# Performance work log

Measured on AMD Instinct MI355X. Metric: run time of the kernel, lower is better.

Reference implementation:

```python
import jax, jax.numpy as jnp
import numpy as np

N_NODES = 50000
N_EDGES = 1600000
N_GRAPHS = 64


def _gcn_conv(x, row, col, ew, W, b, n_nodes):
    # x: [N, Fin] -> [N, Fout]; PyG GCNConv: lin, add self-loops (w=1),
    # symmetric normalization, scatter-add at target (col), + bias.
    x = x @ W
    loop = jnp.arange(n_nodes, dtype=row.dtype)
    r = jnp.concatenate([row, loop])
    c = jnp.concatenate([col, loop])
    w = jnp.concatenate([ew, jnp.ones((n_nodes,), dtype=ew.dtype)])
    deg = jax.ops.segment_sum(w, c, num_segments=n_nodes)
    dinv = jnp.where(deg > 0, jax.lax.rsqrt(jnp.where(deg > 0, deg, 1.0)), 0.0)
    norm = dinv[r] * w * dinv[c]                      # [E+N]
    msg = x[r] * norm[:, None]                        # [E+N, Fout] (dominant traffic)
    out = jax.ops.segment_sum(msg, c, num_segments=n_nodes)
    return out + b


def setup_inputs() -> dict:
    key = jax.random.key(0)
    ks = jax.random.split(key, 12)
    x = jax.random.normal(ks[0], (N_NODES, 128), dtype=jnp.float32)
    edge_index = jax.random.randint(ks[1], (2, N_EDGES), 0, N_NODES, dtype=jnp.int32)
    edge_attr = jax.random.uniform(ks[2], (N_EDGES,), dtype=jnp.float32)
    batch = jnp.sort(jax.random.randint(ks[3], (N_NODES,), 0, N_GRAPHS, dtype=jnp.int32))
    glorot = lambda k, fi, fo: jax.random.normal(k, (fi, fo), jnp.float32) * np.sqrt(2.0 / (fi + fo))
    return {
        "x": x, "edge_index": edge_index, "edge_attr": edge_attr, "batch": batch,
        "W1": glorot(ks[4], 128, 128), "b1": jnp.zeros((128,), jnp.float32),
        "W2": glorot(ks[5], 128, 64), "b2": jnp.zeros((64,), jnp.float32),
        "fc1_W": glorot(ks[6], 64, 128), "fc1_b": jnp.zeros((128,), jnp.float32),
        "fc2_W": glorot(ks[7], 128, 2), "fc2_b": jnp.zeros((2,), jnp.float32),
    }


def reference(x, edge_index, edge_attr, batch, W1, b1, W2, b2, fc1_W, fc1_b, fc2_W, fc2_b):
    row, col = edge_index[0], edge_index[1]
    h = jax.nn.relu(_gcn_conv(x, row, col, edge_attr, W1, b1, N_NODES))
    x1 = jax.nn.relu(_gcn_conv(h, row, col, edge_attr, W2, b2, N_NODES))
    # global mean pool over batch ids
    sums = jax.ops.segment_sum(x1, batch, num_segments=N_GRAPHS)
    cnt = jax.ops.segment_sum(jnp.ones((N_NODES,), x1.dtype), batch, num_segments=N_GRAPHS)
    x2 = sums / jnp.maximum(cnt, 1.0)[:, None]        # [B, 64]
    # dropout is identity in eval mode
    h = jax.nn.relu(x2 @ fc1_W + fc1_b)
    logits = h @ fc2_W + fc2_b                        # [B, 2]
    return jax.nn.log_softmax(logits, axis=1)
```

## Files before the change

kernel.cpp:

```cpp
#include <hip/hip_runtime.h>
#include <hip/hip_bf16.h>


#define CAP 64
#define OVFCAP 8192
#define MAXNR 6400
#define PCH 32
#define BSTR 68
#define KP 136
#define PARTNB 256

typedef float v2f  __attribute__((ext_vector_type(2)));
typedef float f32x4 __attribute__((ext_vector_type(4)));
typedef short bf16x8 __attribute__((ext_vector_type(8)));

__device__ inline unsigned short f2bf(float f) {
    unsigned u = __float_as_uint(f);
    u += 0x7FFFu + ((u >> 16) & 1u);
    return (unsigned short)(u >> 16);
}
__device__ inline void fp8x4_to_f32(unsigned w, float* o) {
    v2f lo = __builtin_amdgcn_cvt_pk_f32_fp8((int)w, false);
    v2f hi = __builtin_amdgcn_cvt_pk_f32_fp8((int)w, true);
    o[0] = lo[0]; o[1] = lo[1]; o[2] = hi[0]; o[3] = hi[1];
}
__device__ inline unsigned f32x4_to_fp8(float a, float b, float c, float d) {
    int w = 0;
    w = __builtin_amdgcn_cvt_pk_fp8_f32(a, b, w, false);
    w = __builtin_amdgcn_cvt_pk_fp8_f32(c, d, w, true);
    return (unsigned)w;
}

__global__ void part_kernel(const int* __restrict__ rows, const int* __restrict__ cols,
                            const float* __restrict__ ew, int* __restrict__ rangeCnt,
                            uint2* __restrict__ rng, int E, int NR, int RSEG,
                            const float* __restrict__ W1, const float* __restrict__ W2,
                            unsigned short* __restrict__ wt1, unsigned short* __restrict__ wt2) {
    const int t = threadIdx.x;
    if (blockIdx.x >= PARTNB) {
        if (blockIdx.x == PARTNB) {
            for (int i = t; i < 128 * 128; i += 256) {
                int c = i >> 7, k = i & 127;
                wt1[c * KP + k] = f2bf(W1[k * 128 + c]);
            }
        } else {
            for (int i = t; i < 64 * 128; i += 256) {
                int c = i >> 7, k = i & 127;
                wt2[c * KP + k] = f2bf(W2[k * 64 + c]);
            }
        }
        return;
    }
    __shared__ int hc[8];
    const int CS = (E + PARTNB - 1) / PARTNB;
    const int e0 = blockIdx.x * CS, e1 = min(e0 + CS, E);
    if (t < 8) hc[t] = 0;
    __syncthreads();
    for (int e = e0 + t; e < e1; e += 256) {
        int r = cols[e] / NR;
        atomicAdd(&hc[r], 1);
    }
    __syncthreads();
    if (t < 8) hc[t] = atomicAdd(&rangeCnt[t], hc[t]);
    __syncthreads();
    for (int e = e0 + t; e < e1; e += 256) {
        int c = cols[e];
        int r = c / NR;
        int q = (int)(ew[e] * 32768.0f);
        if (q > 32767) q = 32767;
        unsigned rec = ((unsigned)rows[e] << 15) | (unsigned)q;
        int pos = atomicAdd(&hc[r], 1);
        if (pos < RSEG) rng[(size_t)r * RSEG + pos] = make_uint2((unsigned)c, rec);
    }
}

__global__ __launch_bounds__(1024)
void hist2_kernel(const uint2* __restrict__ rng, const int* __restrict__ rangeCnt,
                  int* __restrict__ h2d, int* __restrict__ w2d, int NR, int RSEG) {
    __shared__ int hist[MAXNR];
    __shared__ int wsum[MAXNR];
    const int r = blockIdx.x & 7, j = blockIdx.x >> 3;
    const int t = threadIdx.x;
    const int M = min(rangeCnt[r], RSEG);
    const int CS = (M + PCH - 1) / PCH;
    const int e0 = j * CS, e1 = min(e0 + CS, M);
    for (int n = t; n < NR; n += 1024) { hist[n] = 0; wsum[n] = 0; }
    __syncthreads();
    const uint2* lst = rng + (size_t)r * RSEG;
    for (int k = e0 + t; k < e1; k += 1024) {
        unsigned c = lst[k].x - r * NR;
        atomicAdd(&hist[c], 1);
        atomicAdd(&wsum[c], (int)(lst[k].y & 32767u));
    }
    __syncthreads();
    int* dst = h2d + (size_t)(r * PCH + j) * NR;
    int* wdst = w2d + (size_t)(r * PCH + j) * NR;
    for (int n = t; n < NR; n += 1024) { dst[n] = hist[n]; wdst[n] = wsum[n]; }
}

__global__ void scan2_kernel(int* __restrict__ h2d, const int* __restrict__ w2d,
                             int* __restrict__ cnt, float* __restrict__ dinv, int NR, int N) {
    int n = blockIdx.x * 256 + threadIdx.x;
    if (n >= N) return;
    int r = n / NR, c = n - r * NR;
    int* col = h2d + (size_t)(r * PCH) * NR + c;
    const int* wcol = w2d + (size_t)(r * PCH) * NR + c;
    int run = 0;
    long long ws = 0;
    #pragma unroll 8
    for (int j = 0; j < PCH; ++j) {
        int v = col[(size_t)j * NR];
        col[(size_t)j * NR] = run;
        run += v;
        ws += wcol[(size_t)j * NR];
    }
    cnt[n] = run;
    dinv[n] = rsqrtf((float)ws * (1.0f / 32768.0f) + 1.0f);
}

__global__ __launch_bounds__(1024)
void place2_kernel(const uint2* __restrict__ rng, const int* __restrict__ rangeCnt,
                   const int* __restrict__ h2d, unsigned* __restrict__ slot,
                   int4* __restrict__ ovf, int* __restrict__ ovfcnt,
                   int NR, int RSEG) {
    __shared__ int cur[MAXNR];
    const int r = blockIdx.x & 7, j = blockIdx.x >> 3;
    const int t = threadIdx.x;
    const int M = min(rangeCnt[r], RSEG);
    const int CS = (M + PCH - 1) / PCH;
    const int e0 = j * CS, e1 = min(e0 + CS, M);
    const int* src = h2d + (size_t)(r * PCH + j) * NR;
    for (int n = t; n < NR; n += 1024) cur[n] = src[n];
    __syncthreads();
    const uint2* lst = rng + (size_t)r * RSEG;
    for (int k = e0 + t; k < e1; k += 1024) {
        uint2 u2 = lst[k];
        int pos = atomicAdd(&cur[u2.x - r * NR], 1);
        if (pos < CAP) {
            slot[(size_t)u2.x * CAP + pos] = u2.y;
        } else {
            int o = atomicAdd(ovfcnt, 1);
            if (o < OVFCAP)
                ovf[o] = make_int4((int)(u2.y >> 15), (int)u2.x, (int)(u2.y & 32767u), 0);
        }
    }
}

__global__ void place_simple_kernel(const int* __restrict__ rows, const int* __restrict__ cols,
                                    const float* __restrict__ ew, int* __restrict__ cnt,
                                    unsigned* __restrict__ slot, int4* __restrict__ ovf,
                                    int* __restrict__ ovfcnt, int E) {
    int e = blockIdx.x * 256 + threadIdx.x;
    if (e >= E) return;
    int r = rows[e], c = cols[e];
    int q = (int)(ew[e] * 32768.0f);
    if (q > 32767) q = 32767;
    int pos = atomicAdd(&cnt[c], 1);
    if (pos < CAP) {
        slot[(size_t)c * CAP + pos] = ((unsigned)r << 15) | (unsigned)q;
    } else {
        int o = atomicAdd(ovfcnt, 1);
        if (o < OVFCAP) ovf[o] = make_int4(r, c, q, 0);
    }
}

__global__ void degfin_kernel(const unsigned* __restrict__ slot, const int* __restrict__ cnt,
                              const int4* __restrict__ ovf, const int* __restrict__ ovfcnt,
                              float* __restrict__ dinv, int N) {
    const int w = threadIdx.x >> 6, lane = threadIdx.x & 63;
    const int i = blockIdx.x * 4 + w;
    if (i >= N) return;
    int mraw = cnt[i];
    int m = mraw > CAP ? CAP : mraw;
    float v = 0.f;
    if (lane < m) v = (float)(slot[(size_t)i * CAP + lane] & 32767u);
    if (mraw > CAP) {
        int oc = *ovfcnt; if (oc > OVFCAP) oc = OVFCAP;
        for (int k = lane; k < oc; k += 64)
            if (ovf[k].y == i) v += (float)ovf[k].z;
    }
    #pragma unroll
    for (int off = 1; off < 64; off <<= 1) v += __shfl_xor(v, off);
    if (lane == 0) dinv[i] = rsqrtf(v * (1.0f / 32768.0f) + 1.0f);
}

template <int BN, bool AF32>
__global__ __launch_bounds__(256)
void gemm_mfma_kernel(const void* __restrict__ Av, const unsigned short* __restrict__ wt,
                      const float* __restrict__ dinv, unsigned char* __restrict__ outf8,
                      int M) {
    constexpr int CT = BN / 16;
    constexpr int EPS = BN + 4;
    __shared__ unsigned short wl[BN * KP];
    __shared__ float ep[4][16 * EPS];
    const int t = threadIdx.x;
    for (int i = t; i < BN * KP / 8; i += 256)
        ((uint4*)wl)[i] = ((const uint4*)wt)[i];
    __syncthreads();
    const int w = t >> 6, lane = t & 63;
    const int n16 = lane & 15, q = lane >> 4;
    const int rowBase = blockIdx.x * 64 + w * 16;
    int arow = rowBase + n16; if (arow >= M) arow = M - 1;
    f32x4 acc[CT];
    #pragma unroll
    for (int ct = 0; ct < CT; ++ct) acc[ct] = (f32x4){0.f, 0.f, 0.f, 0.f};
    #pragma unroll
    for (int kt = 0; kt < 4; ++kt) {
        bf16x8 af;
        if (AF32) {
            const float* ap = (const float*)Av + (size_t)arow * 128 + kt * 32 + q * 8;
            float4 a0 = *(const float4*)ap;
            float4 a1 = *(const float4*)(ap + 4);
            af[0] = (short)f2bf(a0.x); af[1] = (short)f2bf(a0.y);
            af[2] = (short)f2bf(a0.z); af[3] = (short)f2bf(a0.w);
            af[4] = (short)f2bf(a1.x); af[5] = (short)f2bf(a1.y);
            af[6] = (short)f2bf(a1.z); af[7] = (short)f2bf(a1.w);
        } else {
            af = *(const bf16x8*)((const unsigned short*)Av + (size_t)arow * 128 + kt * 32 + q * 8);
        }
        #pragma unroll
        for (int ct = 0; ct < CT; ++ct) {
            bf16x8 bfr = *(const bf16x8*)&wl[(ct * 16 + n16) * KP + kt * 32 + q * 8];
            acc[ct] = __builtin_amdgcn_mfma_f32_16x16x32_bf16(af, bfr, acc[ct], 0, 0, 0);
        }
    }
    #pragma unroll
    for (int ct = 0; ct < CT; ++ct)
        #pragma unroll
        for (int r = 0; r < 4; ++r)
            ep[w][(q * 4 + r) * EPS + ct * 16 + n16] = acc[ct][r];
    __syncthreads();
    const int lr = lane & 15;
    const int cc = (lane >> 4) * (BN / 4);
    int grow = rowBase + lr;
    if (grow < M) {
        float s = dinv[grow];
        const float* src = &ep[w][lr * EPS + cc];
        #pragma unroll
        for (int u = 0; u < BN / 64; ++u) {
            int col0 = cc + u * 16;
            int slice = col0 >> 6, cw = col0 & 63;
            unsigned w0 = f32x4_to_fp8(src[u*16+ 0]*s, src[u*16+ 1]*s, src[u*16+ 2]*s, src[u*16+ 3]*s);
            unsigned w1 = f32x4_to_fp8(src[u*16+ 4]*s, src[u*16+ 5]*s, src[u*16+ 6]*s, src[u*16+ 7]*s);
            unsigned w2 = f32x4_to_fp8(src[u*16+ 8]*s, src[u*16+ 9]*s, src[u*16+10]*s, src[u*16+11]*s);
            unsigned w3 = f32x4_to_fp8(src[u*16+12]*s, src[u*16+13]*s, src[u*16+14]*s, src[u*16+15]*s);
            *(uint4*)&outf8[((size_t)slice * M + grow) * 64 + cw] = make_uint4(w0, w1, w2, w3);
        }
    }
}

template <int F, int S, bool OB, bool POOL>
__global__ void gather_kernel(const unsigned char* __restrict__ xsb,
                              const unsigned* __restrict__ slot,
                              const int* __restrict__ cnt, const float* __restrict__ dinv,
                              const float* __restrict__ b, const int4* __restrict__ ovf,
                              const int* __restrict__ ovfcnt, void* __restrict__ outv, int N,
                              const int* __restrict__ gbatch, float* __restrict__ gsums,
                              float* __restrict__ gcnt) {
    constexpr int EPN = 4;
    __shared__ unsigned sbkt[16 * BSTR];
    __shared__ float x1s[16 * 68];
    __shared__ int gidl[16];
    const int slice = (S > 1) ? ((int)blockIdx.x % S) : 0;
    const int grp = (S > 1) ? ((int)blockIdx.x / S) : blockIdx.x;
    const int t = threadIdx.x;
    const int node0 = grp * 16;
    {
        int ndl = t >> 4, part = t & 15;
        int snode = node0 + ndl; if (snode >= N) snode = N - 1;
        int sc = cnt[snode]; if (sc > CAP) sc = CAP;
        if (part * 4 < sc)
            *(uint4*)&sbkt[ndl * BSTR + part * 4] =
                *(const uint4*)&slot[(size_t)snode * CAP + part * 4];
    }
    if constexpr (POOL) {
        if (t < 16) {
            int sn = node0 + t;
            gidl[t] = (sn < N) ? gbatch[sn] : -1;
        }
    }
    __syncthreads();
    const int w = t >> 6, lane = t & 63;
    const int cg = lane & 3;
    const int e  = (lane >> 2) & 3;
    const int nd = lane >> 4;
    const int ndl = w * 4 + nd;
    const int i = node0 + ndl;
    const bool iv = (i < N);
    const int ic = iv ? i : 0;
    const uint4* xs4 = (const uint4*)(xsb + (size_t)slice * N * 64);
    int mraw = iv ? cnt[ic] : 0;
    int m = mraw > CAP ? CAP : mraw;
    const unsigned* lb = &sbkt[ndl * BSTR];
    float acc[16] = {};
    int j = e;
    for (; j + EPN < m; j += 2 * EPN) {
        unsigned u0 = lb[j], u1 = lb[j + EPN];
        float c0 = (float)(u0 & 32767u), c1 = (float)(u1 & 32767u);
        uint4 a0 = xs4[(size_t)(u0 >> 15) * 4 + cg];
        uint4 a1 = xs4[(size_t)(u1 >> 15) * 4 + cg];
        float f0[16], f1[16];
        fp8x4_to_f32(a0.x, f0 + 0);  fp8x4_to_f32(a0.y, f0 + 4);
        fp8x4_to_f32(a0.z, f0 + 8);  fp8x4_to_f32(a0.w, f0 + 12);
        fp8x4_to_f32(a1.x, f1 + 0);  fp8x4_to_f32(a1.y, f1 + 4);
        fp8x4_to_f32(a1.z, f1 + 8);  fp8x4_to_f32(a1.w, f1 + 12);
        #pragma unroll
        for (int k = 0; k < 16; ++k) acc[k] += f0[k] * c0 + f1[k] * c1;
    }
    if (j < m) {
        unsigned u = lb[j];
        float c = (float)(u & 32767u);
        uint4 a = xs4[(size_t)(u >> 15) * 4 + cg];
        float f[16];
        fp8x4_to_f32(a.x, f + 0);  fp8x4_to_f32(a.y, f + 4);
        fp8x4_to_f32(a.z, f + 8);  fp8x4_to_f32(a.w, f + 12);
        #pragma unroll
        for (int k = 0; k < 16; ++k) acc[k] += f[k] * c;
    }
    if (mraw > CAP) {
        int oc = *ovfcnt; if (oc > OVFCAP) oc = OVFCAP;
        for (int k = e; k < oc; k += EPN) {
            int4 r4 = ovf[k];
            if (r4.y == i) {
                float c = (float)r4.z;
                uint4 a = xs4[(size_t)r4.x * 4 + cg];
                float f[16];
                fp8x4_to_f32(a.x, f + 0);  fp8x4_to_f32(a.y, f + 4);
                fp8x4_to_f32(a.z, f + 8);  fp8x4_to_f32(a.w, f + 12);
                #pragma unroll
                for (int kk = 0; kk < 16; ++kk) acc[kk] += f[kk] * c;
            }
        }
    }
    #pragma unroll
    for (int k = 0; k < 16; ++k) {
        acc[k] += __shfl_xor(acc[k], 4);
        acc[k] += __shfl_xor(acc[k], 8);
    }
    if (e == 0 && iv) {
        float d = dinv[i];
        float sa = d * (1.0f / 32768.0f);
        uint4 sv = xs4[(size_t)i * 4 + cg];
        float sf[16];
        fp8x4_to_f32(sv.x, sf + 0);  fp8x4_to_f32(sv.y, sf + 4);
        fp8x4_to_f32(sv.z, sf + 8);  fp8x4_to_f32(sv.w, sf + 12);
        const float* bb = &b[slice * 64 + cg * 16];
        float o[16];
        #pragma unroll
        for (int k = 0; k < 16; ++k)
            o[k] = fmaxf(acc[k] * sa + sf[k] * d + bb[k], 0.f);
        if (OB) {
            unsigned short* dst = (unsigned short*)outv + (size_t)i * F + slice * 64 + cg * 16;
            unsigned pw[8];
            #pragma unroll
            for (int k = 0; k < 8; ++k)
                pw[k] = (unsigned)f2bf(o[2 * k]) | ((unsigned)f2bf(o[2 * k + 1]) << 16);
            *(uint4*)&dst[0] = make_uint4(pw[0], pw[1], pw[2], pw[3]);
            *(uint4*)&dst[8] = make_uint4(pw[4], pw[5], pw[6], pw[7]);
        } else if constexpr (!POOL) {
            float* dst = (float*)outv + (size_t)i * F + slice * 64 + cg * 16;
            *(float4*)&dst[0]  = make_float4(o[0], o[1], o[2], o[3]);
            *(float4*)&dst[4]  = make_float4(o[4], o[5], o[6], o[7]);
            *(float4*)&dst[8]  = make_float4(o[8], o[9], o[10], o[11]);
            *(float4*)&dst[12] = make_float4(o[12], o[13], o[14], o[15]);
        } else {
            float* dst = &x1s[ndl * 68 + cg * 16];
            *(float4*)&dst[0]  = make_float4(o[0], o[1], o[2], o[3]);
            *(float4*)&dst[4]  = make_float4(o[4], o[5], o[6], o[7]);
            *(float4*)&dst[8]  = make_float4(o[8], o[9], o[10], o[11]);
            *(float4*)&dst[12] = make_float4(o[12], o[13], o[14], o[15]);
        }
    }
    if constexpr (POOL) {
        __syncthreads();
        if (t < 64) {
            const int f = t;
            float run = 0.f; int gcur = -1;
            #pragma unroll 4
            for (int n = 0; n < 16; ++n) {
                int g = gidl[n];
                if (g < 0) break;
                if (g != gcur) {
                    if (gcur >= 0) atomicAdd(&gsums[gcur * 64 + f], run);
                    run = 0.f; gcur = g;
                }
                run += x1s[n * 68 + f];
            }
            if (gcur >= 0) atomicAdd(&gsums[gcur * 64 + f], run);
        } else if (t == 64) {
            float rc = 0.f; int gcur = -1;
            for (int n = 0; n < 16; ++n) {
                int g = gidl[n];
                if (g < 0) break;
                if (g != gcur) {
                    if (gcur >= 0) atomicAdd(&gcnt[gcur], rc);
                    rc = 0.f; gcur = g;
                }
                rc += 1.f;
            }
            if (gcur >= 0) atomicAdd(&gcnt[gcur], rc);
        }
    }
}

__global__ void head_kernel(const float* __restrict__ sums, const float* __restrict__ cnt,
                            const float* __restrict__ fc1W, const float* __restrict__ fc1b,
                            const float* __restrict__ fc2W, const float* __restrict__ fc2b,
                            float* __restrict__ out) {
    __shared__ float x2s[64];
    __shared__ float hs[128];
    __shared__ float lg[2];
    const int g = blockIdx.x;
    const int t = threadIdx.x;
    if (t < 64) {
        float c = fmaxf(cnt[g], 1.f);
        x2s[t] = sums[g * 64 + t] / c;
    }
    __syncthreads();
    {
        float a = fc1b[t];
        #pragma unroll 8
        for (int j = 0; j < 64; ++j) a += x2s[j] * fc1W[j * 128 + t];
        hs[t] = fmaxf(a, 0.f);
    }
    __syncthreads();
    {
        int m = t >> 6, l = t & 63;
        float p = hs[l] * fc2W[l * 2 + m] + hs[l + 64] * fc2W[(l + 64) * 2 + m];
        #pragma unroll
        for (int off = 1; off < 64; off <<= 1) p += __shfl_xor(p, off);
        if (l == 0) lg[m] = p + fc2b[m];
    }
    __syncthreads();
    if (t == 0) {
        float l0 = lg[0], l1 = lg[1];
        float mx = fmaxf(l0, l1);
        float lse = mx + logf(expf(l0 - mx) + expf(l1 - mx));
        out[g * 2 + 0] = l0 - lse;
        out[g * 2 + 1] = l1 - lse;
    }
}

extern "C" void kernel_launch(void* const* d_in, const int* in_sizes, int n_in,
                              void* d_out, int out_size, void* d_ws, size_t ws_size,
                              hipStream_t stream) {
    const float* x      = (const float*)d_in[0];
    const int*   eidx   = (const int*)d_in[1];
    const float* ew     = (const float*)d_in[2];
    const int*   batch  = (const int*)d_in[3];
    const float* W1     = (const float*)d_in[4];
    const float* b1     = (const float*)d_in[5];
    const float* W2     = (const float*)d_in[6];
    const float* b2     = (const float*)d_in[7];
    const float* fc1W   = (const float*)d_in[8];
    const float* fc1b   = (const float*)d_in[9];
    const float* fc2W   = (const float*)d_in[10];
    const float* fc2b   = (const float*)d_in[11];
    float* out = (float*)d_out;

    const int N = in_sizes[3];
    const int E = in_sizes[2];
    const int G = 64;
    const int* rows = eidx;
    const int* cols = eidx + E;
    const int NR = (N + 7) / 8;
    const int RSEG = E / 8 + 32768;

    float* ws = (float*)d_ws;
    size_t off = 0;
    auto alloc = [&](size_t n) { float* p = ws + off; off += (n + 15) & ~(size_t)15; return p; };
    float*    sums     = alloc(64 * 64);
    float*    cntf     = alloc(16);
    int*      ovfcnt   = (int*)alloc(16);
    int*      rangeCnt = (int*)alloc(16);
    int*      cnt      = (int*)alloc(N);
    size_t zfloats = off;
    float*    dinv   = alloc(N);
    unsigned short* wt1 = (unsigned short*)alloc(128 * KP / 2 + 16);
    unsigned short* wt2 = (unsigned short*)alloc(64 * KP / 2 + 16);
    unsigned* slot   = (unsigned*)alloc((size_t)N * CAP);
    int4*     ovf    = (int4*)alloc((size_t)OVFCAP * 4);
    float*    bufA   = alloc((size_t)N * 128);
    float*    bufB   = alloc((size_t)N * 128);
    int*            h2d   = (int*)bufA;
    int*            w2d   = h2d + (size_t)8 * PCH * NR;
    unsigned char*  xw1f8 = (unsigned char*)bufA;
    unsigned char*  xw2f8 = (unsigned char*)bufA;
    uint2*          rng   = (uint2*)bufB;
    unsigned short* hbf   = (unsigned short*)bufB;
    (void)ws_size;

    hipMemsetAsync(d_ws, 0, zfloats * sizeof(float), stream);

    if (NR <= MAXNR) {
        part_kernel<<<PARTNB + 2, 256, 0, stream>>>(rows, cols, ew, rangeCnt, rng, E, NR, RSEG,
                                                    W1, W2, wt1, wt2);
        hist2_kernel<<<8 * PCH, 1024, 0, stream>>>(rng, rangeCnt, h2d, w2d, NR, RSEG);
        scan2_kernel<<<(N + 255) / 256, 256, 0, stream>>>(h2d, w2d, cnt, dinv, NR, N);
        place2_kernel<<<8 * PCH, 1024, 0, stream>>>(rng, rangeCnt, h2d, slot, ovf, ovfcnt, NR, RSEG);
    } else {
        part_kernel<<<PARTNB + 2, 256, 0, stream>>>(rows, cols, ew, rangeCnt, rng, E, NR, RSEG,
                                                    W1, W2, wt1, wt2);
        place_simple_kernel<<<(E + 255) / 256, 256, 0, stream>>>(rows, cols, ew, cnt, slot, ovf, ovfcnt, E);
        degfin_kernel<<<(N + 3) / 4, 256, 0, stream>>>(slot, cnt, ovf, ovfcnt, dinv, N);
    }

    gemm_mfma_kernel<128, true><<<(N + 63) / 64, 256, 0, stream>>>(x, wt1, dinv, xw1f8, N);
    gather_kernel<128, 2, true, false><<<((N + 15) / 16) * 2, 256, 0, stream>>>(
        xw1f8, slot, cnt, dinv, b1, ovf, ovfcnt, hbf, N, nullptr, nullptr, nullptr);

    gemm_mfma_kernel<64, false><<<(N + 63) / 64, 256, 0, stream>>>(hbf, wt2, dinv, xw2f8, N);
    gather_kernel<64, 1, false, true><<<(N + 15) / 16, 256, 0, stream>>>(
        xw2f8, slot, cnt, dinv, b2, ovf, ovfcnt, nullptr, N, batch, sums, cntf);

    head_kernel<<<G, 128, 0, stream>>>(sums, cntf, fc1W, fc1b, fc2W, fc2b, out);
}
```

Measured before the change: 239.6 us.

## Replace hist/scan/place pipeline with single global-atomic placement pass

Drops the three-kernel counting-sort bucketing pass (per-chunk LDS histogram, column scan, LDS-cursor placement). It becomes one place kernel that takes slot positions and accumulates integer edge-weight sums with global atomics on cnt and wsum. dinv is no longer stored and is recomputed from wsum wherever it is read, in the gemm and gather epilogues. This cuts two launches and the h2d/w2d traffic, but brings contended global atomics. Slot order within a node also becomes nondeterministic.

```diff
diff --git a/kernel.cpp b/kernel.cpp
--- a/kernel.cpp
+++ b/kernel.cpp
@@ -5,7 +5,7 @@
 #define CAP 64
 #define OVFCAP 8192
 #define MAXNR 6400
-#define PCH 32
+#define PCH 128
 #define BSTR 68
 #define KP 136
 #define PARTNB 256
@@ -29,6 +29,9 @@
     w = __builtin_amdgcn_cvt_pk_fp8_f32(a, b, w, false);
     w = __builtin_amdgcn_cvt_pk_fp8_f32(c, d, w, true);
     return (unsigned)w;
+}
+__device__ inline float dinv_of(int ws) {
+    return rsqrtf((float)ws * (1.0f / 32768.0f) + 1.0f);
 }
 
 __global__ void part_kernel(const int* __restrict__ rows, const int* __restrict__ cols,
@@ -74,80 +77,36 @@
     }
 }
 
-__global__ __launch_bounds__(1024)
-void hist2_kernel(const uint2* __restrict__ rng, const int* __restrict__ rangeCnt,
-                  int* __restrict__ h2d, int* __restrict__ w2d, int NR, int RSEG) {
-    __shared__ int hist[MAXNR];
-    __shared__ int wsum[MAXNR];
+__global__ __launch_bounds__(256)
+void place_kernel(const uint2* __restrict__ rng, const int* __restrict__ rangeCnt,
+                  int* __restrict__ cnt, int* __restrict__ wsum,
+                  unsigned* __restrict__ slot, int4* __restrict__ ovf,
+                  int* __restrict__ ovfcnt, int NR, int RSEG) {
     const int r = blockIdx.x & 7, j = blockIdx.x >> 3;
     const int t = threadIdx.x;
     const int M = min(rangeCnt[r], RSEG);
     const int CS = (M + PCH - 1) / PCH;
     const int e0 = j * CS, e1 = min(e0 + CS, M);
-    for (int n = t; n < NR; n += 1024) { hist[n] = 0; wsum[n] = 0; }
-    __syncthreads();
     const uint2* lst = rng + (size_t)r * RSEG;
-    for (int k = e0 + t; k < e1; k += 1024) {
-        unsigned c = lst[k].x - r * NR;
-        atomicAdd(&hist[c], 1);
-        atomicAdd(&wsum[c], (int)(lst[k].y & 32767u));
-    }
-    __syncthreads();
-    int* dst = h2d + (size_t)(r * PCH + j) * NR;
-    int* wdst = w2d + (size_t)(r * PCH + j) * NR;
-    for (int n = t; n < NR; n += 1024) { dst[n] = hist[n]; wdst[n] = wsum[n]; }
-}
-
-__global__ void scan2_kernel(int* __restrict__ h2d, const int* __restrict__ w2d,
-                             int* __restrict__ cnt, float* __restrict__ dinv, int NR, int N) {
-    int n = blockIdx.x * 256 + threadIdx.x;
-    if (n >= N) return;
-    int r = n / NR, c = n - r * NR;
-    int* col = h2d + (size_t)(r * PCH) * NR + c;
-    const int* wcol = w2d + (size_t)(r * PCH) * NR + c;
-    int run = 0;
-    long long ws = 0;
-    #pragma unroll 8
-    for (int j = 0; j < PCH; ++j) {
-        int v = col[(size_t)j * NR];
-        col[(size_t)j * NR] = run;
-        run += v;
-        ws += wcol[(size_t)j * NR];
-    }
-    cnt[n] = run;
-    dinv[n] = rsqrtf((float)ws * (1.0f / 32768.0f) + 1.0f);
-}
-
-__global__ __launch_bounds__(1024)
-void place2_kernel(const uint2* __restrict__ rng, const int* __restrict__ rangeCnt,
-                   const int* __restrict__ h2d, unsigned* __restrict__ slot,
-                   int4* __restrict__ ovf, int* __restrict__ ovfcnt,
-                   int NR, int RSEG) {
-    __shared__ int cur[MAXNR];
-    const int r = blockIdx.x & 7, j = blockIdx.x >> 3;
-    const int t = threadIdx.x;
-    const int M = min(rangeCnt[r], RSEG);
-    const int CS = (M + PCH - 1) / PCH;
-    const int e0 = j * CS, e1 = min(e0 + CS, M);
-    const int* src = h2d + (size_t)(r * PCH + j) * NR;
-    for (int n = t; n < NR; n += 1024) cur[n] = src[n];
-    __syncthreads();
-    const uint2* lst = rng + (size_t)r * RSEG;
-    for (int k = e0 + t; k < e1; k += 1024) {
+    for (int k = e0 + t; k < e1; k += 256) {
         uint2 u2 = lst[k];
-        int pos = atomicAdd(&cur[u2.x - r * NR], 1);
+        unsigned c = u2.x;
+        int q = (int)(u2.y & 32767u);
+        int pos = atomicAdd(&cnt[c], 1);
+        atomicAdd(&wsum[c], q);
         if (pos < CAP) {
-            slot[(size_t)u2.x * CAP + pos] = u2.y;
+            slot[(size_t)c * CAP + pos] = u2.y;
         } else {
             int o = atomicAdd(ovfcnt, 1);
             if (o < OVFCAP)
-                ovf[o] = make_int4((int)(u2.y >> 15), (int)u2.x, (int)(u2.y & 32767u), 0);
+                ovf[o] = make_int4((int)(u2.y >> 15), (int)c, q, 0);
         }
     }
 }
 
 __global__ void place_simple_kernel(const int* __restrict__ rows, const int* __restrict__ cols,
                                     const float* __restrict__ ew, int* __restrict__ cnt,
+                                    int* __restrict__ wsum,
                                     unsigned* __restrict__ slot, int4* __restrict__ ovf,
                                     int* __restrict__ ovfcnt, int E) {
     int e = blockIdx.x * 256 + threadIdx.x;
@@ -156,6 +115,7 @@
     int q = (int)(ew[e] * 32768.0f);
     if (q > 32767) q = 32767;
     int pos = atomicAdd(&cnt[c], 1);
+    atomicAdd(&wsum[c], q);
     if (pos < CAP) {
         slot[(size_t)c * CAP + pos] = ((unsigned)r << 15) | (unsigned)q;
     } else {
@@ -164,30 +124,10 @@
     }
 }
 
-__global__ void degfin_kernel(const unsigned* __restrict__ slot, const int* __restrict__ cnt,
-                              const int4* __restrict__ ovf, const int* __restrict__ ovfcnt,
-                              float* __restrict__ dinv, int N) {
-    const int w = threadIdx.x >> 6, lane = threadIdx.x & 63;
-    const int i = blockIdx.x * 4 + w;
-    if (i >= N) return;
-    int mraw = cnt[i];
-    int m = mraw > CAP ? CAP : mraw;
-    float v = 0.f;
-    if (lane < m) v = (float)(slot[(size_t)i * CAP + lane] & 32767u);
-    if (mraw > CAP) {
-        int oc = *ovfcnt; if (oc > OVFCAP) oc = OVFCAP;
-        for (int k = lane; k < oc; k += 64)
-            if (ovf[k].y == i) v += (float)ovf[k].z;
-    }
-    #pragma unroll
-    for (int off = 1; off < 64; off <<= 1) v += __shfl_xor(v, off);
-    if (lane == 0) dinv[i] = rsqrtf(v * (1.0f / 32768.0f) + 1.0f);
-}
-
 template <int BN, bool AF32>
 __global__ __launch_bounds__(256)
 void gemm_mfma_kernel(const void* __restrict__ Av, const unsigned short* __restrict__ wt,
-                      const float* __restrict__ dinv, unsigned char* __restrict__ outf8,
+                      const int* __restrict__ wsum, unsigned char* __restrict__ outf8,
                       int M) {
     constexpr int CT = BN / 16;
     constexpr int EPS = BN + 4;
@@ -234,7 +174,7 @@
     const int cc = (lane >> 4) * (BN / 4);
     int grow = rowBase + lr;
     if (grow < M) {
-        float s = dinv[grow];
+        float s = dinv_of(wsum[grow]);
         const float* src = &ep[w][lr * EPS + cc];
         #pragma unroll
         for (int u = 0; u < BN / 64; ++u) {
@@ -252,7 +192,7 @@
 template <int F, int S, bool OB, bool POOL>
 __global__ void gather_kernel(const unsigned char* __restrict__ xsb,
                               const unsigned* __restrict__ slot,
-                              const int* __restrict__ cnt, const float* __restrict__ dinv,
+                              const int* __restrict__ cnt, const int* __restrict__ wsum,
                               const float* __restrict__ b, const int4* __restrict__ ovf,
                               const int* __restrict__ ovfcnt, void* __restrict__ outv, int N,
                               const int* __restrict__ gbatch, float* __restrict__ gsums,
@@ -338,7 +278,7 @@
         acc[k] += __shfl_xor(acc[k], 8);
     }
     if (e == 0 && iv) {
-        float d = dinv[i];
+        float d = dinv_of(wsum[i]);
         float sa = d * (1.0f / 32768.0f);
         uint4 sv = xs4[(size_t)i * 4 + cg];
         float sf[16];
@@ -474,16 +414,14 @@
     int*      ovfcnt   = (int*)alloc(16);
     int*      rangeCnt = (int*)alloc(16);
     int*      cnt      = (int*)alloc(N);
+    int*      wsum     = (int*)alloc(N);
     size_t zfloats = off;
-    float*    dinv   = alloc(N);
     unsigned short* wt1 = (unsigned short*)alloc(128 * KP / 2 + 16);
     unsigned short* wt2 = (unsigned short*)alloc(64 * KP / 2 + 16);
     unsigned* slot   = (unsigned*)alloc((size_t)N * CAP);
     int4*     ovf    = (int4*)alloc((size_t)OVFCAP * 4);
     float*    bufA   = alloc((size_t)N * 128);
     float*    bufB   = alloc((size_t)N * 128);
-    int*            h2d   = (int*)bufA;
-    int*            w2d   = h2d + (size_t)8 * PCH * NR;
     unsigned char*  xw1f8 = (unsigned char*)bufA;
     unsigned char*  xw2f8 = (unsigned char*)bufA;
     uint2*          rng   = (uint2*)bufB;
@@ -495,23 +433,20 @@
     if (NR <= MAXNR) {
         part_kernel<<<PARTNB + 2, 256, 0, stream>>>(rows, cols, ew, rangeCnt, rng, E, NR, RSEG,
                                                     W1, W2, wt1, wt2);
-        hist2_kernel<<<8 * PCH, 1024, 0, stream>>>(rng, rangeCnt, h2d, w2d, NR, RSEG);
-        scan2_kernel<<<(N + 255) / 256, 256, 0, stream>>>(h2d, w2d, cnt, dinv, NR, N);
-        place2_kernel<<<8 * PCH, 1024, 0, stream>>>(rng, rangeCnt, h2d, slot, ovf, ovfcnt, NR, RSEG);
+        place_kernel<<<8 * PCH, 256, 0, stream>>>(rng, rangeCnt, cnt, wsum, slot, ovf, ovfcnt, NR, RSEG);
     } else {
         part_kernel<<<PARTNB + 2, 256, 0, stream>>>(rows, cols, ew, rangeCnt, rng, E, NR, RSEG,
                                                     W1, W2, wt1, wt2);
-        place_simple_kernel<<<(E + 255) / 256, 256, 0, stream>>>(rows, cols, ew, cnt, slot, ovf, ovfcnt, E);
-        degfin_kernel<<<(N + 3) / 4, 256, 0, stream>>>(slot, cnt, ovf, ovfcnt, dinv, N);
-    }
-
-    gemm_mfma_kernel<128, true><<<(N + 63) / 64, 256, 0, stream>>>(x, wt1, dinv, xw1f8, N);
+        place_simple_kernel<<<(E + 255) / 256, 256, 0, stream>>>(rows, cols, ew, cnt, wsum, slot, ovf, ovfcnt, E);
+    }
+
+    gemm_mfma_kernel<128, true><<<(N + 63) / 64, 256, 0, stream>>>(x, wt1, wsum, xw1f8, N);
     gather_kernel<128, 2, true, false><<<((N + 15) / 16) * 2, 256, 0, stream>>>(
-        xw1f8, slot, cnt, dinv, b1, ovf, ovfcnt, hbf, N, nullptr, nullptr, nullptr);
-
-    gemm_mfma_kernel<64, false><<<(N + 63) / 64, 256, 0, stream>>>(hbf, wt2, dinv, xw2f8, N);
+        xw1f8, slot, cnt, wsum, b1, ovf, ovfcnt, hbf, N, nullptr, nullptr, nullptr);
+
+    gemm_mfma_kernel<64, false><<<(N + 63) / 64, 256, 0, stream>>>(hbf, wt2, wsum, xw2f8, N);
     gather_kernel<64, 1, false, true><<<(N + 15) / 16, 256, 0, stream>>>(
-        xw2f8, slot, cnt, dinv, b2, ovf, ovfcnt, nullptr, N, batch, sums, cntf);
+        xw2f8, slot, cnt, wsum, b2, ovf, ovfcnt, nullptr, N, batch, sums, cntf);
 
     head_kernel<<<G, 128, 0, stream>>>(sums, cntf, fc1W, fc1b, fc2W, fc2b, out);
 }
```

Result: slower. 333.5 us (+39.2%).
